# Kernel tuning notes

Hardware: AMD Instinct MI355X
Metric: run time of the kernel (lower is better)

## Reference

```python
import jax, jax.numpy as jnp
import numpy as np


def setup_inputs() -> dict:
    key = jax.random.key(0)
    k1, k2 = jax.random.split(key, 2)
    B, K, N, Fdim = 32, 8, 2048, 64
    regime_probs = jax.random.uniform(k1, (B, K), dtype=jnp.float32)
    factor_loadings = jax.random.normal(k2, (K, N, Fdim), dtype=jnp.float32)
    specific_risk = jnp.ones((K, N), dtype=jnp.float32)
    return {
        "regime_probs": regime_probs,
        "factor_loadings": factor_loadings,
        "specific_risk": specific_risk,
    }


def reference(regime_probs, factor_loadings, specific_risk):
    # Handle [B, K, T] -> take last time step (as in original)
    if regime_probs.ndim == 3:
        regime_probs = regime_probs[:, :, -1]
    K, N, _ = factor_loadings.shape
    # Per-regime covariance: F_k F_k^T + diag(specific_risk_k^2)  -> [K, N, N]
    cov_k = jnp.einsum("knf,kmf->knm", factor_loadings, factor_loadings)
    eye = jnp.eye(N, dtype=cov_k.dtype)
    cov_k = cov_k + eye[None, :, :] * (specific_risk ** 2)[:, :, None]
    # Regime-weighted mixture per batch element -> [B, N, N]
    return jnp.einsum("bk,knm->bnm", regime_probs, cov_k)
```

## Files before the change

### kernel.cpp

```cpp
#include <hip/hip_runtime.h>

#define NDIM 2048
#define FDIM 64
#define KDIM 8
#define BDIM 32
#define TILE 64
#define BFROW 72
#define FROW  68

typedef __attribute__((ext_vector_type(8))) short short8;
typedef __attribute__((ext_vector_type(4))) float f32x4;

static __device__ __forceinline__ unsigned short f2bf(float x) {
    unsigned u = __float_as_uint(x);
    return (unsigned short)((u + 0x7fffu + ((u >> 16) & 1u)) >> 16);
}

__global__ __launch_bounds__(256, 2) void rfm_fused_mfma(
    const float* __restrict__ p, const float* __restrict__ L,
    const float* __restrict__ sr, float* __restrict__ out)
{
    __shared__ float pl[BDIM * KDIM];
    __shared__ __align__(16) char smem[4 * TILE * FROW * 4];

    unsigned short* An = (unsigned short*)smem;
    unsigned short* Am = An + TILE * BFROW;

    const int n0 = blockIdx.y * TILE;
    const int m0 = blockIdx.x * TILE;
    const int t  = threadIdx.x;
    const int lane = t & 63;
    const int w   = t >> 6;
    const int wr  = w >> 1;
    const int wc  = w & 1;
    const int l15 = lane & 15;
    const int l4  = lane >> 4;

    pl[t] = p[t];

    f32x4 acc[KDIM][2][2];
    #pragma unroll
    for (int k = 0; k < KDIM; ++k)
        #pragma unroll
        for (int ti = 0; ti < 2; ++ti)
            #pragma unroll
            for (int tj = 0; tj < 2; ++tj)
                acc[k][ti][tj] = (f32x4){0.f, 0.f, 0.f, 0.f};

    #pragma unroll
    for (int k = 0; k < KDIM; ++k) {
        const float* Lk = L + (size_t)k * (NDIM * FDIM);

        #pragma unroll
        for (int r = 0; r < 4; ++r) {
            const int idx = t + r * 256;
            const int row = idx >> 4;
            const int fc  = (idx & 15) << 2;
            const float4 va = *(const float4*)&Lk[(size_t)(n0 + row) * FDIM + fc];
            const float4 vb = *(const float4*)&Lk[(size_t)(m0 + row) * FDIM + fc];
            ushort4 ua, ub;
            ua.x = f2bf(va.x); ua.y = f2bf(va.y); ua.z = f2bf(va.z); ua.w = f2bf(va.w);
            ub.x = f2bf(vb.x); ub.y = f2bf(vb.y); ub.z = f2bf(vb.z); ub.w = f2bf(vb.w);
            *(ushort4*)&An[row * BFROW + fc] = ua;
            *(ushort4*)&Am[row * BFROW + fc] = ub;
        }
        __syncthreads();

        short8 af[2][2], bv[2][2];
        #pragma unroll
        for (int ti = 0; ti < 2; ++ti)
            #pragma unroll
            for (int s = 0; s < 2; ++s) {
                af[ti][s] = *(const short8*)
                    &An[(wr * 32 + ti * 16 + l15) * BFROW + s * 32 + l4 * 8];
                bv[ti][s] = *(const short8*)
                    &Am[(wc * 32 + ti * 16 + l15) * BFROW + s * 32 + l4 * 8];
            }
        #pragma unroll
        for (int ti = 0; ti < 2; ++ti)
            #pragma unroll
            for (int tj = 0; tj < 2; ++tj)
                #pragma unroll
                for (int s = 0; s < 2; ++s)
                    acc[k][ti][tj] = __builtin_amdgcn_mfma_f32_16x16x32_bf16(
                        af[ti][s], bv[tj][s], acc[k][ti][tj], 0, 0, 0);
        __syncthreads();
    }

    if (n0 == m0 && wr == wc) {
        #pragma unroll
        for (int k = 0; k < KDIM; ++k)
            #pragma unroll
            for (int ti = 0; ti < 2; ++ti)
                #pragma unroll
                for (int reg = 0; reg < 4; ++reg) {
                    const int row = l4 * 4 + reg;
                    if (row == l15) {
                        const float q = sr[k * NDIM + n0 + wr * 32 + ti * 16 + row];
                        acc[k][ti][ti][reg] += q * q;
                    }
                }
    }

    float* const P0 = (float*)smem;
    float* const P1 = (float*)(smem + 1 * TILE * FROW * 4);
    float* const P2 = (float*)(smem + 2 * TILE * FROW * 4);
    float* const P3 = (float*)(smem + 3 * TILE * FROW * 4);
    float* const Pp[4] = { P0, P1, P2, P3 };

    const int tx = t & 15;
    const int ty = t >> 4;
    const size_t NN = (size_t)NDIM * NDIM;
    float* obase = out + (size_t)n0 * NDIM + m0;

    #pragma unroll 1
    for (int b = 0; b < BDIM; b += 4) {
        float pv[4][KDIM];
        #pragma unroll
        for (int u = 0; u < 4; ++u)
            #pragma unroll
            for (int k = 0; k < KDIM; ++k)
                pv[u][k] = pl[(b + u) * KDIM + k];

        #pragma unroll
        for (int ti = 0; ti < 2; ++ti)
            #pragma unroll
            for (int tj = 0; tj < 2; ++tj)
                #pragma unroll
                for (int reg = 0; reg < 4; ++reg) {
                    const int rl = wr * 32 + ti * 16 + l4 * 4 + reg;
                    const int cl = wc * 32 + tj * 16 + l15;
                    #pragma unroll
                    for (int u = 0; u < 4; ++u) {
                        float v = 0.0f;
                        #pragma unroll
                        for (int k = 0; k < KDIM; ++k)
                            v += pv[u][k] * acc[k][ti][tj][reg];
                        Pp[u][rl * FROW + cl] = v;
                    }
                }
        asm volatile("s_waitcnt lgkmcnt(0)" ::: "memory");
        __builtin_amdgcn_s_barrier();
        __builtin_amdgcn_sched_barrier(0);

        #pragma unroll
        for (int q = 0; q < 4; ++q) {
            const int row = ty + 16 * q;
            #pragma unroll
            for (int u = 0; u < 4; ++u) {
                const f32x4 wv = *(const f32x4*)&Pp[u][row * FROW + tx * 4];
                *(f32x4*)(obase + (size_t)(b + u) * NN
                                + (size_t)row * NDIM + tx * 4) = wv;
            }
        }
        asm volatile("s_waitcnt lgkmcnt(0)" ::: "memory");
        __builtin_amdgcn_s_barrier();
        __builtin_amdgcn_sched_barrier(0);
    }
}

extern "C" void kernel_launch(void* const* d_in, const int* in_sizes, int n_in,
                              void* d_out, int out_size, void* d_ws, size_t ws_size,
                              hipStream_t stream)
{
    const float* p  = (const float*)d_in[0];
    const float* L  = (const float*)d_in[1];
    const float* sr = (const float*)d_in[2];
    float* out = (float*)d_out;

    dim3 grid(NDIM / TILE, NDIM / TILE);
    hipLaunchKernelGGL(rfm_fused_mfma, grid, dim3(256), 0, stream,
                       p, L, sr, out);
}
```

Before: 125.6 us.

## Shrink output tile to 32x32, raise occupancy, use nontemporal output stores

Reduces the block tile from 64x64 to 32x32 so each wave computes a single 16x16 MFMA tile per regime, cutting accumulator registers and allowing four blocks per CU. Output staging buffers shrink accordingly, and global writes of the large [B,N,N] result use nontemporal stores to avoid polluting caches. The trade-off is doubled factor-loading reads and conversions across more blocks, and shorter contiguous write segments per row.

```diff
diff --git a/kernel.cpp b/kernel.cpp
--- a/kernel.cpp
+++ b/kernel.cpp
@@ -4,9 +4,9 @@
 #define FDIM 64
 #define KDIM 8
 #define BDIM 32
-#define TILE 64
+#define TILE 32
 #define BFROW 72
-#define FROW  68
+#define FROW2 36
 
 typedef __attribute__((ext_vector_type(8))) short short8;
 typedef __attribute__((ext_vector_type(4))) float f32x4;
@@ -16,15 +16,19 @@
     return (unsigned short)((u + 0x7fffu + ((u >> 16) & 1u)) >> 16);
 }
 
-__global__ __launch_bounds__(256, 2) void rfm_fused_mfma(
+__global__ __launch_bounds__(256, 4) void rfm_fused_mfma(
     const float* __restrict__ p, const float* __restrict__ L,
     const float* __restrict__ sr, float* __restrict__ out)
 {
     __shared__ float pl[BDIM * KDIM];
-    __shared__ __align__(16) char smem[4 * TILE * FROW * 4];
+    __shared__ __align__(16) char smem[4 * TILE * FROW2 * 4];
 
-    unsigned short* An = (unsigned short*)smem;
-    unsigned short* Am = An + TILE * BFROW;
+    unsigned short* const An = (unsigned short*)smem;
+    unsigned short* const Am = An + TILE * BFROW;
+    float* const Pp0 = (float*)smem;
+    float* const Pp1 = Pp0 + TILE * FROW2;
+    float* const Pp2 = Pp1 + TILE * FROW2;
+    float* const Pp3 = Pp2 + TILE * FROW2;
 
     const int n0 = blockIdx.y * TILE;
     const int m0 = blockIdx.x * TILE;
@@ -38,21 +42,16 @@
 
     pl[t] = p[t];
 
-    f32x4 acc[KDIM][2][2];
+    f32x4 acc[KDIM];
     #pragma unroll
-    for (int k = 0; k < KDIM; ++k)
-        #pragma unroll
-        for (int ti = 0; ti < 2; ++ti)
-            #pragma unroll
-            for (int tj = 0; tj < 2; ++tj)
-                acc[k][ti][tj] = (f32x4){0.f, 0.f, 0.f, 0.f};
+    for (int k = 0; k < KDIM; ++k) acc[k] = (f32x4){0.f, 0.f, 0.f, 0.f};
 
     #pragma unroll
     for (int k = 0; k < KDIM; ++k) {
         const float* Lk = L + (size_t)k * (NDIM * FDIM);
 
         #pragma unroll
-        for (int r = 0; r < 4; ++r) {
+        for (int r = 0; r < 2; ++r) {
             const int idx = t + r * 256;
             const int row = idx >> 4;
             const int fc  = (idx & 15) << 2;
@@ -66,24 +65,16 @@
         }
         __syncthreads();
 
-        short8 af[2][2], bv[2][2];
+        short8 af[2], bv[2];
         #pragma unroll
-        for (int ti = 0; ti < 2; ++ti)
-            #pragma unroll
-            for (int s = 0; s < 2; ++s) {
-                af[ti][s] = *(const short8*)
-                    &An[(wr * 32 + ti * 16 + l15) * BFROW + s * 32 + l4 * 8];
-                bv[ti][s] = *(const short8*)
-                    &Am[(wc * 32 + ti * 16 + l15) * BFROW + s * 32 + l4 * 8];
-            }
+        for (int s = 0; s < 2; ++s) {
+            af[s] = *(const short8*)&An[(wr * 16 + l15) * BFROW + s * 32 + l4 * 8];
+            bv[s] = *(const short8*)&Am[(wc * 16 + l15) * BFROW + s * 32 + l4 * 8];
+        }
         #pragma unroll
-        for (int ti = 0; ti < 2; ++ti)
-            #pragma unroll
-            for (int tj = 0; tj < 2; ++tj)
-                #pragma unroll
-                for (int s = 0; s < 2; ++s)
-                    acc[k][ti][tj] = __builtin_amdgcn_mfma_f32_16x16x32_bf16(
-                        af[ti][s], bv[tj][s], acc[k][ti][tj], 0, 0, 0);
+        for (int s = 0; s < 2; ++s)
+            acc[k] = __builtin_amdgcn_mfma_f32_16x16x32_bf16(
+                af[s], bv[s], acc[k], 0, 0, 0);
         __syncthreads();
     }
 
@@ -91,67 +82,47 @@
         #pragma unroll
         for (int k = 0; k < KDIM; ++k)
             #pragma unroll
-            for (int ti = 0; ti < 2; ++ti)
-                #pragma unroll
-                for (int reg = 0; reg < 4; ++reg) {
-                    const int row = l4 * 4 + reg;
-                    if (row == l15) {
-                        const float q = sr[k * NDIM + n0 + wr * 32 + ti * 16 + row];
-                        acc[k][ti][ti][reg] += q * q;
-                    }
+            for (int reg = 0; reg < 4; ++reg) {
+                if (l4 * 4 + reg == l15) {
+                    const float q = sr[k * NDIM + n0 + wr * 16 + l15];
+                    acc[k][reg] += q * q;
                 }
+            }
     }
 
-    float* const P0 = (float*)smem;
-    float* const P1 = (float*)(smem + 1 * TILE * FROW * 4);
-    float* const P2 = (float*)(smem + 2 * TILE * FROW * 4);
-    float* const P3 = (float*)(smem + 3 * TILE * FROW * 4);
-    float* const Pp[4] = { P0, P1, P2, P3 };
-
-    const int tx = t & 15;
-    const int ty = t >> 4;
     const size_t NN = (size_t)NDIM * NDIM;
-    float* obase = out + (size_t)n0 * NDIM + m0;
+    const int rbrow = t >> 3;
+    const int rbc4  = (t & 7) * 4;
+    const int rl = wr * 16 + l4 * 4;
+    const int cl = wc * 16 + l15;
+    float* const obase = out + (size_t)(n0 + rbrow) * NDIM + (m0 + rbc4);
+    float* const Parr[4] = { Pp0, Pp1, Pp2, Pp3 };
 
     #pragma unroll 1
     for (int b = 0; b < BDIM; b += 4) {
-        float pv[4][KDIM];
         #pragma unroll
-        for (int u = 0; u < 4; ++u)
+        for (int u = 0; u < 4; ++u) {
+            float pb[KDIM];
             #pragma unroll
-            for (int k = 0; k < KDIM; ++k)
-                pv[u][k] = pl[(b + u) * KDIM + k];
-
-        #pragma unroll
-        for (int ti = 0; ti < 2; ++ti)
+            for (int k = 0; k < KDIM; ++k) pb[k] = pl[(b + u) * KDIM + k];
+            float* const Pu = Parr[u];
             #pragma unroll
-            for (int tj = 0; tj < 2; ++tj)
+            for (int reg = 0; reg < 4; ++reg) {
+                float v = 0.0f;
                 #pragma unroll
-                for (int reg = 0; reg < 4; ++reg) {
-                    const int rl = wr * 32 + ti * 16 + l4 * 4 + reg;
-                    const int cl = wc * 32 + tj * 16 + l15;
-                    #pragma unroll
-                    for (int u = 0; u < 4; ++u) {
-                        float v = 0.0f;
-                        #pragma unroll
-                        for (int k = 0; k < KDIM; ++k)
-                            v += pv[u][k] * acc[k][ti][tj][reg];
-                        Pp[u][rl * FROW + cl] = v;
-                    }
-                }
+                for (int k = 0; k < KDIM; ++k) v += pb[k] * acc[k][reg];
+                Pu[(rl + reg) * FROW2 + cl] = v;
+            }
+        }
         asm volatile("s_waitcnt lgkmcnt(0)" ::: "memory");
         __builtin_amdgcn_s_barrier();
         __builtin_amdgcn_sched_barrier(0);
 
         #pragma unroll
-        for (int q = 0; q < 4; ++q) {
-            const int row = ty + 16 * q;
-            #pragma unroll
-            for (int u = 0; u < 4; ++u) {
-                const f32x4 wv = *(const f32x4*)&Pp[u][row * FROW + tx * 4];
-                *(f32x4*)(obase + (size_t)(b + u) * NN
-                                + (size_t)row * NDIM + tx * 4) = wv;
-            }
+        for (int u = 0; u < 4; ++u) {
+            const f32x4 wv = *(const f32x4*)&Parr[u][rbrow * FROW2 + rbc4];
+            __builtin_nontemporal_store(wv,
+                (f32x4*)(obase + (size_t)(b + u) * NN));
         }
         asm volatile("s_waitcnt lgkmcnt(0)" ::: "memory");
         __builtin_amdgcn_s_barrier();
```

After: 129.9 us. +3.5%, slower.
